# Kernel tuning notes

Measured on AMD Instinct MI355X. Metric: run time of the kernel, lower is better.

The kernel has to match this reference:

```python
import math
import jax, jax.numpy as jnp
import numpy as np

N_NODES = 50000
N_EDGES = 600000
IN_CH = 64      # in_channels == out_channels (residual requires it)
HEADS = 2
C = 64          # per-head dim == out_channels
HC = HEADS * C  # 128
EDGE_DIM = 32


def setup_inputs() -> dict:
    key = jax.random.key(0)
    ks = jax.random.split(key, 12)
    s = 0.05
    return {
        "x": jax.random.normal(ks[0], (N_NODES, IN_CH), jnp.float32),
        "edge_index": jax.random.randint(ks[1], (2, N_EDGES), 0, N_NODES, dtype=jnp.int64),
        "edge_attr": jax.random.normal(ks[2], (N_EDGES, EDGE_DIM), jnp.float32),
        "Wq": s * jax.random.normal(ks[3], (IN_CH, HC), jnp.float32),
        "bq": jnp.zeros((HC,), jnp.float32),
        "Wk": s * jax.random.normal(ks[4], (IN_CH, HC), jnp.float32),
        "bk": jnp.zeros((HC,), jnp.float32),
        "Wv": s * jax.random.normal(ks[5], (IN_CH, HC), jnp.float32),
        "bv": jnp.zeros((HC,), jnp.float32),
        "We": s * jax.random.normal(ks[6], (EDGE_DIM, HC), jnp.float32),
        "Wp": s * jax.random.normal(ks[7], (HC, IN_CH), jnp.float32),
        "bp": jnp.zeros((IN_CH,), jnp.float32),
        "ln1_g": jnp.ones((IN_CH,), jnp.float32),
        "ln1_b": jnp.zeros((IN_CH,), jnp.float32),
        "ln2_g": jnp.ones((IN_CH,), jnp.float32),
        "ln2_b": jnp.zeros((IN_CH,), jnp.float32),
        "W1": s * jax.random.normal(ks[8], (IN_CH, IN_CH), jnp.float32),
        "b1": jnp.zeros((IN_CH,), jnp.float32),
        "W2": s * jax.random.normal(ks[9], (IN_CH, IN_CH), jnp.float32),
        "b2": jnp.zeros((IN_CH,), jnp.float32),
    }


def _layernorm(x, g, b, eps=1e-5):
    m = jnp.mean(x, axis=-1, keepdims=True)
    v = jnp.mean(jnp.square(x - m), axis=-1, keepdims=True)
    return (x - m) / jnp.sqrt(v + eps) * g + b


def reference(x, edge_index, edge_attr, Wq, bq, Wk, bk, Wv, bv, We, Wp, bp,
              ln1_g, ln1_b, ln2_g, ln2_b, W1, b1, W2, b2):
    n = x.shape[0]
    residual = x
    h = _layernorm(x, ln1_g, ln1_b)
    q = (h @ Wq + bq).reshape(n, HEADS, C)
    k = (h @ Wk + bk).reshape(n, HEADS, C)
    v = (h @ Wv + bv).reshape(n, HEADS, C)

    src, tgt = edge_index[0], edge_index[1]
    e = (edge_attr @ We).reshape(-1, HEADS, C)   # (E,H,C)
    qi = q[tgt]                                  # (E,H,C) gather by target
    kj = k[src] + e
    vj = v[src] + e

    alpha = jnp.sum(qi * kj, axis=-1) / math.sqrt(C)            # (E,H)
    amax = jax.ops.segment_max(alpha, tgt, num_segments=n)      # (N,H)
    ex = jnp.exp(alpha - amax[tgt])
    den = jax.ops.segment_sum(ex, tgt, num_segments=n)          # (N,H)
    a = ex / (den[tgt] + 1e-8)                                  # (E,H)

    agg = jax.ops.segment_sum(a[:, :, None] * vj, tgt, num_segments=n)  # (N,H,C)
    out = agg.reshape(n, HC) @ Wp + bp
    out = out + residual                        # in_channels == out_channels

    res2 = out
    o = _layernorm(out, ln2_g, ln2_b)
    o = jax.nn.gelu(o @ W1 + b1, approximate=False) @ W2 + b2
    return o + res2
```

## Files before the change

### kernel.cpp

```cpp
#include <hip/hip_runtime.h>
#include <math.h>
#include <stdint.h>


typedef float f32x4 __attribute__((ext_vector_type(4)));
typedef __bf16 bf16x8 __attribute__((ext_vector_type(8)));
typedef unsigned int u32x4 __attribute__((ext_vector_type(4)));

#define WP_S 152
#define W1_OFF 9728
#define W2_OFF 15360
#define W_TOT 20992
#define H_S 72

__device__ __forceinline__ unsigned pack_bf16(float2 v) {
    unsigned a = __builtin_bit_cast(unsigned, v.x);
    unsigned b = __builtin_bit_cast(unsigned, v.y);
    a = (a + 0x7FFFu + ((a >> 16) & 1u)) >> 16;
    b = (b + 0x7FFFu + ((b >> 16) & 1u)) >> 16;
    return a | (b << 16);
}
__device__ __forceinline__ float2 unpack_bf16(unsigned p) {
    float x = __builtin_bit_cast(float, p << 16);
    float y = __builtin_bit_cast(float, p & 0xFFFF0000u);
    return make_float2(x, y);
}
__device__ __forceinline__ unsigned short bf16r(float x) {
    unsigned u = __builtin_bit_cast(unsigned, x);
    return (unsigned short)((u + 0x7FFFu + ((u >> 16) & 1u)) >> 16);
}

__device__ __forceinline__ f32x4 mfma16(bf16x8 a, bf16x8 b, f32x4 c) {
    return __builtin_amdgcn_mfma_f32_16x16x32_bf16(a, b, c, 0, 0, 0);
}
__device__ __forceinline__ bf16x8 frag_ld(const unsigned short* p) {
    return __builtin_bit_cast(bf16x8, *(const u32x4*)p);
}

__global__ void k_pre(const float* __restrict__ Wq, const float* __restrict__ Wk,
                      const float* __restrict__ Wv, const float* __restrict__ We,
                      const float* __restrict__ Wp, const float* __restrict__ W1,
                      const float* __restrict__ W2, const float* __restrict__ bq,
                      const float* __restrict__ bk, const float* __restrict__ bv,
                      float* __restrict__ Wqt, float* __restrict__ Wkt,
                      float* __restrict__ Wvt, float* __restrict__ Wet,
                      unsigned short* __restrict__ wsW, float* __restrict__ bqt,
                      float* __restrict__ bkt, float* __restrict__ bvt,
                      int* __restrict__ deg, int n) {
    int idx = blockIdx.x * 256 + threadIdx.x;
    for (int i = idx; i < n; i += gridDim.x * 256) deg[i] = 0;
    if (idx < 8192) {
        int cin = idx >> 7, j = idx & 127, h = j >> 6, c = j & 63;
        int dst = cin * 128 + c * 2 + h;
        Wqt[dst] = Wq[idx];
        Wkt[dst] = Wk[idx];
        Wvt[dst] = Wv[idx];
        int o = idx >> 7, k = idx & 127;
        wsW[o * WP_S + k] = bf16r(Wp[((k & 1) * 64 + (k >> 1)) * 64 + o]);
    }
    if (idx < 4096) {
        int d = idx >> 7, j = idx & 127, h = j >> 6, c = j & 63;
        Wet[(d * 64 + c) * 2 + h] = We[idx];
        int o = idx >> 6, k = idx & 63;
        wsW[W1_OFF + o * 88 + k] = bf16r(W1[k * 64 + o]);
        wsW[W2_OFF + o * 88 + k] = bf16r(W2[k * 64 + o]);
    }
    if (idx < 128) {
        int h = idx >> 6, c = idx & 63;
        bqt[c * 2 + h] = bq[idx];
        bkt[c * 2 + h] = bk[idx];
        bvt[c * 2 + h] = bv[idx];
    }
}

__global__ __launch_bounds__(256) void k_bucket(
    const int* __restrict__ ei, int* __restrict__ deg,
    int2* __restrict__ bucket2, int E, int n) {
    int e = blockIdx.x * 256 + threadIdx.x;
    if (e >= E) return;
    int src = ei[e], tgt = ei[E + e];
    src = min(max(src, 0), n - 1);
    tgt = min(max(tgt, 0), n - 1);
    int slot = atomicAdd(&deg[tgt], 1);
    if (slot < 64) bucket2[(size_t)tgt * 64 + slot] = make_int2(e, src);
}

__global__ __launch_bounds__(256) void k_qkv(
    const float* __restrict__ x,
    const float* __restrict__ Wqt, const float* __restrict__ Wkt, const float* __restrict__ Wvt,
    const float* __restrict__ bqt, const float* __restrict__ bkt, const float* __restrict__ bvt,
    const float* __restrict__ g1, const float* __restrict__ b1,
    const float* __restrict__ We,
    unsigned* __restrict__ qx, unsigned* __restrict__ kbf,
    unsigned* __restrict__ vbf, int n) {
    __shared__ __align__(16) float hT[4][64][8];
    __shared__ __align__(16) float qs[4][2][8][64];
    int wave = threadIdx.x >> 6, lane = threadIdx.x & 63;
    int node0 = blockIdx.x * 32 + wave * 8;
    if (node0 >= n) return;

    int b = lane >> 3, t = lane & 7;
    int nodeb = node0 + b;
    float4 xa = make_float4(0.f, 0.f, 0.f, 0.f), xb = xa;
    if (nodeb < n) {
        const float4* xp = (const float4*)(x + (size_t)nodeb * 64 + t * 8);
        xa = xp[0]; xb = xp[1];
    }
    float s1 = (xa.x + xa.y) + (xa.z + xa.w) + (xb.x + xb.y) + (xb.z + xb.w);
    float s2 = xa.x*xa.x + xa.y*xa.y + xa.z*xa.z + xa.w*xa.w
             + xb.x*xb.x + xb.y*xb.y + xb.z*xb.z + xb.w*xb.w;
#pragma unroll
    for (int m = 1; m < 8; m <<= 1) {
        s1 += __shfl_xor(s1, m);
        s2 += __shfl_xor(s2, m);
    }
    float mean = s1 * 0.015625f;
    float var  = s2 * 0.015625f - mean * mean;
    float rstd = rsqrtf(var + 1e-5f);
    float4 ga = ((const float4*)(g1 + t * 8))[0];
    float4 gb = ((const float4*)(g1 + t * 8))[1];
    float4 ba = ((const float4*)(b1 + t * 8))[0];
    float4 bb = ((const float4*)(b1 + t * 8))[1];
    float hv[8];
    hv[0] = (xa.x - mean) * rstd * ga.x + ba.x;
    hv[1] = (xa.y - mean) * rstd * ga.y + ba.y;
    hv[2] = (xa.z - mean) * rstd * ga.z + ba.z;
    hv[3] = (xa.w - mean) * rstd * ga.w + ba.w;
    hv[4] = (xb.x - mean) * rstd * gb.x + bb.x;
    hv[5] = (xb.y - mean) * rstd * gb.y + bb.y;
    hv[6] = (xb.z - mean) * rstd * gb.z + bb.z;
    hv[7] = (xb.w - mean) * rstd * gb.w + bb.w;
#pragma unroll
    for (int j = 0; j < 8; ++j) hT[wave][t * 8 + j][b] = hv[j];

    const float2* Wq2 = (const float2*)Wqt;
    const float2* Wk2 = (const float2*)Wkt;
    const float2* Wv2 = (const float2*)Wvt;
    float2 bqv = ((const float2*)bqt)[lane];
    float2 bkv = ((const float2*)bkt)[lane];
    float2 bvv = ((const float2*)bvt)[lane];
    float2 qa[8], ka[8], va[8];
#pragma unroll
    for (int nb = 0; nb < 8; ++nb) { qa[nb] = bqv; ka[nb] = bkv; va[nb] = bvv; }

#pragma unroll 4
    for (int cin = 0; cin < 64; ++cin) {
        float2 w_q = Wq2[cin * 64 + lane];
        float2 w_k = Wk2[cin * 64 + lane];
        float2 w_v = Wv2[cin * 64 + lane];
        const float4* hp = (const float4*)&hT[wave][cin][0];
        float4 h0 = hp[0], h1 = hp[1];
        float hs[8] = {h0.x, h0.y, h0.z, h0.w, h1.x, h1.y, h1.z, h1.w};
#pragma unroll
        for (int nb = 0; nb < 8; ++nb) {
            qa[nb].x += hs[nb] * w_q.x; qa[nb].y += hs[nb] * w_q.y;
            ka[nb].x += hs[nb] * w_k.x; ka[nb].y += hs[nb] * w_k.y;
            va[nb].x += hs[nb] * w_v.x; va[nb].y += hs[nb] * w_v.y;
        }
    }

#pragma unroll
    for (int nb = 0; nb < 8; ++nb) {
        int nd = node0 + nb;
        if (nd < n) {
            qx[(size_t)nd * 128 + lane] = pack_bf16(qa[nb]);
            kbf[(size_t)nd * 64 + lane] = pack_bf16(ka[nb]);
            vbf[(size_t)nd * 64 + lane] = pack_bf16(va[nb]);
        }
        qs[wave][0][nb][lane] = qa[nb].x;
        qs[wave][1][nb][lane] = qa[nb].y;
    }

    int hh = lane >> 5, d = lane & 31;
    const float4* Wr = (const float4*)(We + d * 128 + hh * 64);
    float wqa[8] = {0.f, 0.f, 0.f, 0.f, 0.f, 0.f, 0.f, 0.f};
#pragma unroll 4
    for (int c4 = 0; c4 < 16; ++c4) {
        float4 w = Wr[c4];
#pragma unroll
        for (int nb = 0; nb < 8; ++nb) {
            float4 qv = *(const float4*)&qs[wave][hh][nb][c4 * 4];
            wqa[nb] += w.x * qv.x + w.y * qv.y + w.z * qv.z + w.w * qv.w;
        }
    }
#pragma unroll
    for (int nb = 0; nb < 8; ++nb)
        if (node0 + nb < n)
            ((float*)qx)[(size_t)(node0 + nb) * 128 + 64 + d * 2 + hh] = wqa[nb];
}

__global__ __launch_bounds__(256) void k_attn(
    const unsigned* __restrict__ qx, const unsigned* __restrict__ kbf,
    const unsigned* __restrict__ vbf, const float* __restrict__ edge_attr,
    const int* __restrict__ deg, const int2* __restrict__ bucket2,
    const float* __restrict__ Wet,
    unsigned* __restrict__ agg, int n, int E) {
    __shared__ __align__(16) unsigned sq[4][64];
    __shared__ __align__(16) float swq[4][64];
    __shared__ __align__(16) float srow[4][64];
    __shared__ __align__(16) float2 sv[4][64];
    int wave = threadIdx.x >> 6, lane = threadIdx.x & 63;
    int node = blockIdx.x * 4 + wave;
    if (node >= n) return;
    int sub = lane >> 4, l = lane & 15;

    sq[wave][lane] = qx[(size_t)node * 128 + lane];
    swq[wave][lane] = ((const float*)qx)[(size_t)node * 128 + 64 + lane];

    int dcount = min(deg[node], 64);
    int eid_l = 0, src_l = 0;
    if (lane < dcount) {
        int2 b = bucket2[(size_t)node * 64 + lane];
        eid_l = min(max(b.x, 0), E - 1);
        src_l = min(max(b.y, 0), n - 1);
    }

    uint4 qq = *(const uint4*)&sq[wave][l * 4];
    float4 w4 = *(const float4*)&swq[wave][l * 4];
    float2 q0 = unpack_bf16(qq.x), q1 = unpack_bf16(qq.y),
           q2 = unpack_bf16(qq.z), q3 = unpack_bf16(qq.w);

    float accA[4] = {0.f, 0.f, 0.f, 0.f}, accB[4] = {0.f, 0.f, 0.f, 0.f};
    float aS0 = 0.f, aS1 = 0.f, bS0 = 0.f, bS1 = 0.f;
    float den0 = 0.f, den1 = 0.f;

    for (int i = 0; i < dcount; i += 4) {
        int j = i + sub;
        bool valid = j < dcount;
        int jj = j & 63;
        int ej = __shfl(eid_l, jj);
        int sj = __shfl(src_l, jj);
        uint4 kk = ((const uint4*)kbf)[(size_t)sj * 16 + l];
        uint4 vv = ((const uint4*)vbf)[(size_t)sj * 16 + l];
        float2 a2 = ((const float2*)edge_attr)[(size_t)ej * 16 + l];
        float2 k0 = unpack_bf16(kk.x), k1 = unpack_bf16(kk.y),
               k2 = unpack_bf16(kk.z), k3 = unpack_bf16(kk.w);
        float r0 = q0.x * k0.x + q1.x * k1.x + q2.x * k2.x + q3.x * k3.x
                 + w4.x * a2.x + w4.z * a2.y;
        float r1 = q0.y * k0.y + q1.y * k1.y + q2.y * k2.y + q3.y * k3.y
                 + w4.y * a2.x + w4.w * a2.y;
#pragma unroll
        for (int m = 1; m < 16; m <<= 1) {
            r0 += __shfl_xor(r0, m);
            r1 += __shfl_xor(r1, m);
        }
        float ex0 = valid ? __expf(r0 * 0.125f) : 0.f;
        float ex1 = valid ? __expf(r1 * 0.125f) : 0.f;
        float2 v0 = unpack_bf16(vv.x), v1 = unpack_bf16(vv.y),
               v2 = unpack_bf16(vv.z), v3 = unpack_bf16(vv.w);
        accA[0] += ex0 * v0.x; accB[0] += ex1 * v0.y;
        accA[1] += ex0 * v1.x; accB[1] += ex1 * v1.y;
        accA[2] += ex0 * v2.x; accB[2] += ex1 * v2.y;
        accA[3] += ex0 * v3.x; accB[3] += ex1 * v3.y;
        aS0 += ex0 * a2.x; aS1 += ex1 * a2.x;
        bS0 += ex0 * a2.y; bS1 += ex1 * a2.y;
        den0 += ex0; den1 += ex1;
    }

#pragma unroll
    for (int m = 16; m < 64; m <<= 1) {
#pragma unroll
        for (int j = 0; j < 4; ++j) {
            accA[j] += __shfl_xor(accA[j], m);
            accB[j] += __shfl_xor(accB[j], m);
        }
        aS0 += __shfl_xor(aS0, m); aS1 += __shfl_xor(aS1, m);
        bS0 += __shfl_xor(bS0, m); bS1 += __shfl_xor(bS1, m);
        den0 += __shfl_xor(den0, m); den1 += __shfl_xor(den1, m);
    }

    if (sub == 0) {
        srow[wave][4 * l + 0] = aS0;
        srow[wave][4 * l + 1] = aS1;
        srow[wave][4 * l + 2] = bS0;
        srow[wave][4 * l + 3] = bS1;
        sv[wave][4 * l + 0] = make_float2(accA[0], accB[0]);
        sv[wave][4 * l + 1] = make_float2(accA[1], accB[1]);
        sv[wave][4 * l + 2] = make_float2(accA[2], accB[2]);
        sv[wave][4 * l + 3] = make_float2(accA[3], accB[3]);
    }

    float B0 = 0.f, B1 = 0.f;
    const float2* We2 = (const float2*)Wet;
    const float2* S2 = (const float2*)srow[wave];
#pragma unroll
    for (int d = 0; d < 32; ++d) {
        float2 w = We2[d * 64 + lane];
        float2 s = S2[d];
        B0 += w.x * s.x;
        B1 += w.y * s.y;
    }
    float2 av2 = sv[wave][lane];
    float r0 = 1.0f / (den0 + 1e-8f);
    float r1 = 1.0f / (den1 + 1e-8f);
    agg[(size_t)node * 64 + lane] =
        pack_bf16(make_float2((av2.x + B0) * r0, (av2.y + B1) * r1));
}

__global__ __launch_bounds__(256) void k_post(
    const unsigned short* __restrict__ aggbf,
    const unsigned short* __restrict__ wsW,
    const float* __restrict__ bp, const float* __restrict__ x,
    const float* __restrict__ g2, const float* __restrict__ b2,
    const float* __restrict__ b1f, const float* __restrict__ b2f,
    float* __restrict__ out, int n) {
    __shared__ __align__(16) unsigned short sW[W_TOT];
    __shared__ __align__(16) unsigned short hb[4][2][16 * H_S];
    int tid = threadIdx.x;
    for (int i = tid; i < W_TOT / 8; i += 256)
        ((u32x4*)sW)[i] = ((const u32x4*)wsW)[i];
    __syncthreads();

    int wave = tid >> 6, lane = tid & 63;
    int cl = lane & 15, kg = lane >> 4;
    unsigned short* h2 = hb[wave][0];
    unsigned short* h3 = hb[wave][1];

    float bp_c[4], g2_c[4], b2_c[4], b1_c[4], bf2_c[4];
#pragma unroll
    for (int t = 0; t < 4; ++t) {
        int c = t * 16 + cl;
        bp_c[t] = bp[c];
        g2_c[t] = g2[c];
        b2_c[t] = b2[c];
        b1_c[t] = b1f[c];
        bf2_c[t] = b2f[c];
    }

    int wid = blockIdx.x * 4 + wave;
    int nbatch = (n + 15) >> 4;
    int nwaves = gridDim.x * 4;
    for (int bt = wid; bt < nbatch; bt += nwaves) {
        int node0 = bt * 16;

        f32x4 acc1[4];
#pragma unroll
        for (int t = 0; t < 4; ++t) acc1[t] = (f32x4){0.f, 0.f, 0.f, 0.f};
        int arow = min(node0 + cl, n - 1);
#pragma unroll
        for (int s = 0; s < 4; ++s) {
            bf16x8 af = frag_ld(aggbf + (size_t)arow * 128 + s * 32 + kg * 8);
#pragma unroll
            for (int t = 0; t < 4; ++t) {
                bf16x8 bf = frag_ld(sW + (t * 16 + cl) * WP_S + s * 32 + kg * 8);
                acc1[t] = mfma16(af, bf, acc1[t]);
            }
        }
#pragma unroll
        for (int t = 0; t < 4; ++t) {
#pragma unroll
            for (int j = 0; j < 4; ++j) {
                int nd = min(node0 + kg * 4 + j, n - 1);
                acc1[t][j] += bp_c[t] + x[(size_t)nd * 64 + t * 16 + cl];
            }
        }

        float mean[4], rstd[4];
#pragma unroll
        for (int j = 0; j < 4; ++j) {
            float s1 = acc1[0][j] + acc1[1][j] + acc1[2][j] + acc1[3][j];
            float s2 = acc1[0][j] * acc1[0][j] + acc1[1][j] * acc1[1][j]
                     + acc1[2][j] * acc1[2][j] + acc1[3][j] * acc1[3][j];
#pragma unroll
            for (int m = 1; m < 16; m <<= 1) {
                s1 += __shfl_xor(s1, m);
                s2 += __shfl_xor(s2, m);
            }
            mean[j] = s1 * 0.015625f;
            float var = s2 * 0.015625f - mean[j] * mean[j];
            rstd[j] = rsqrtf(var + 1e-5f);
        }
#pragma unroll
        for (int t = 0; t < 4; ++t)
#pragma unroll
            for (int j = 0; j < 4; ++j) {
                float v = (acc1[t][j] - mean[j]) * rstd[j] * g2_c[t] + b2_c[t];
                h2[(kg * 4 + j) * H_S + t * 16 + cl] = bf16r(v);
            }
        asm volatile("s_waitcnt lgkmcnt(0)" ::: "memory");

        f32x4 acc2[4];
#pragma unroll
        for (int t = 0; t < 4; ++t)
            acc2[t] = (f32x4){b1_c[t], b1_c[t], b1_c[t], b1_c[t]};
#pragma unroll
        for (int s = 0; s < 2; ++s) {
            bf16x8 af = frag_ld(h2 + cl * H_S + s * 32 + kg * 8);
#pragma unroll
            for (int t = 0; t < 4; ++t) {
                bf16x8 bf = frag_ld(sW + W1_OFF + (t * 16 + cl) * 88 + s * 32 + kg * 8);
                acc2[t] = mfma16(af, bf, acc2[t]);
            }
        }
#pragma unroll
        for (int t = 0; t < 4; ++t)
#pragma unroll
            for (int j = 0; j < 4; ++j) {
                float v = acc2[t][j];
                v = 0.5f * v * (1.0f + erff(v * 0.70710678118654752f));
                h3[(kg * 4 + j) * H_S + t * 16 + cl] = bf16r(v);
            }
        asm volatile("s_waitcnt lgkmcnt(0)" ::: "memory");

        f32x4 acc3[4];
#pragma unroll
        for (int t = 0; t < 4; ++t) {
            acc3[t] = acc1[t];
#pragma unroll
            for (int j = 0; j < 4; ++j) acc3[t][j] += bf2_c[t];
        }
#pragma unroll
        for (int s = 0; s < 2; ++s) {
            bf16x8 af = frag_ld(h3 + cl * H_S + s * 32 + kg * 8);
#pragma unroll
            for (int t = 0; t < 4; ++t) {
                bf16x8 bf = frag_ld(sW + W2_OFF + (t * 16 + cl) * 88 + s * 32 + kg * 8);
                acc3[t] = mfma16(af, bf, acc3[t]);
            }
        }
#pragma unroll
        for (int t = 0; t < 4; ++t)
#pragma unroll
            for (int j = 0; j < 4; ++j) {
                int r = node0 + kg * 4 + j;
                if (r < n) out[(size_t)r * 64 + t * 16 + cl] = acc3[t][j];
            }
    }
}

extern "C" void kernel_launch(void* const* d_in, const int* in_sizes, int n_in,
                              void* d_out, int out_size, void* d_ws, size_t ws_size,
                              hipStream_t stream) {
    const float* x  = (const float*)d_in[0];
    const int*   ei = (const int*)d_in[1];
    const float* ea = (const float*)d_in[2];
    const float* Wq = (const float*)d_in[3];
    const float* bq = (const float*)d_in[4];
    const float* Wk = (const float*)d_in[5];
    const float* bk = (const float*)d_in[6];
    const float* Wv = (const float*)d_in[7];
    const float* bv = (const float*)d_in[8];
    const float* We = (const float*)d_in[9];
    const float* Wp = (const float*)d_in[10];
    const float* bp = (const float*)d_in[11];
    const float* g1 = (const float*)d_in[12];
    const float* b1 = (const float*)d_in[13];
    const float* g2 = (const float*)d_in[14];
    const float* b2 = (const float*)d_in[15];
    const float* W1 = (const float*)d_in[16];
    const float* b1f = (const float*)d_in[17];
    const float* W2 = (const float*)d_in[18];
    const float* b2f = (const float*)d_in[19];

    const int n = in_sizes[0] / 64;
    const int E = in_sizes[2] / 32;

    char* p = (char*)d_ws;
    unsigned* qx = (unsigned*)p; p += (size_t)n * 128 * 4;
    unsigned* kbf = (unsigned*)p; p += (size_t)n * 64 * 4;
    unsigned* vbf = (unsigned*)p; p += (size_t)n * 64 * 4;
    int* deg   = (int*)p;   p += (size_t)n * 4;
    p = (char*)(((uintptr_t)p + 15) & ~(uintptr_t)15);
    int2* bucket2 = (int2*)p; p += (size_t)n * 64 * 8;
    unsigned* aggbf = (unsigned*)p; p += (size_t)n * 64 * 4;
    float* Wqt = (float*)p; p += 8192 * 4;
    float* Wkt = (float*)p; p += 8192 * 4;
    float* Wvt = (float*)p; p += 8192 * 4;
    float* Wet = (float*)p; p += 4096 * 4;
    unsigned short* wsW = (unsigned short*)p; p += W_TOT * 2;
    float* bqt = (float*)p; p += 128 * 4;
    float* bkt = (float*)p; p += 128 * 4;
    float* bvt = (float*)p; p += 128 * 4;

    k_pre<<<196, 256, 0, stream>>>(Wq, Wk, Wv, We, Wp, W1, W2, bq, bk, bv,
                                   Wqt, Wkt, Wvt, Wet, wsW, bqt, bkt, bvt,
                                   deg, n);
    k_bucket<<<(E + 255) / 256, 256, 0, stream>>>(ei, deg, bucket2, E, n);
    k_qkv<<<(n + 31) / 32, 256, 0, stream>>>(x, Wqt, Wkt, Wvt, bqt, bkt, bvt,
                                             g1, b1, We, qx, kbf, vbf, n);
    k_attn<<<(n + 3) / 4, 256, 0, stream>>>(qx, kbf, vbf, ea, deg, bucket2,
                                            Wet, aggbf, n, E);
    int nb16 = (n + 15) >> 4;
    int blocks = (nb16 + 3) / 4;
    if (blocks > 391) blocks = 391;
    k_post<<<blocks, 256, 0, stream>>>((const unsigned short*)aggbf, wsW,
                                       bp, x, g2, b2, b1f, b2f,
                                       (float*)d_out, n);
}
```

Baseline: 364.3 us.

## Fold We into Wp, software-pipeline edge gathers, and shrink bucket storage

Precomputes We·Wp so the attention kernel writes the per-head weighted edge-attribute sums (64 extra bf16 values per node) and the projection MFMA loop absorbs them, removing the per-node 32x64 We multiply and its shared-memory staging from k_attn. The edge loop now prefetches the next group's K, V and edge_attr rows while computing the current one. Source indices are stored as 16-bit values in a separate array to cut bucket traffic. In exchange the aggregate buffer grows from 128 to 192 bf16 per node, k_post does 6 instead of 4 K-steps, and the 16-bit source index only works while n fits in 65536.

```diff
diff --git a/kernel.cpp b/kernel.cpp
--- a/kernel.cpp
+++ b/kernel.cpp
@@ -7,10 +7,10 @@
 typedef __bf16 bf16x8 __attribute__((ext_vector_type(8)));
 typedef unsigned int u32x4 __attribute__((ext_vector_type(4)));
 
-#define WP_S 152
-#define W1_OFF 9728
-#define W2_OFF 15360
-#define W_TOT 20992
+#define WPM_S 200
+#define W1_OFF 12800
+#define W2_OFF 18432
+#define W_TOT 24064
 #define H_S 72
 
 __device__ __forceinline__ unsigned pack_bf16(float2 v) {
@@ -43,7 +43,7 @@
                       const float* __restrict__ W2, const float* __restrict__ bq,
                       const float* __restrict__ bk, const float* __restrict__ bv,
                       float* __restrict__ Wqt, float* __restrict__ Wkt,
-                      float* __restrict__ Wvt, float* __restrict__ Wet,
+                      float* __restrict__ Wvt,
                       unsigned short* __restrict__ wsW, float* __restrict__ bqt,
                       float* __restrict__ bkt, float* __restrict__ bvt,
                       int* __restrict__ deg, int n) {
@@ -56,14 +56,17 @@
         Wkt[dst] = Wk[idx];
         Wvt[dst] = Wv[idx];
         int o = idx >> 7, k = idx & 127;
-        wsW[o * WP_S + k] = bf16r(Wp[((k & 1) * 64 + (k >> 1)) * 64 + o]);
+        wsW[o * WPM_S + k] = bf16r(Wp[((k & 1) * 64 + (k >> 1)) * 64 + o]);
     }
     if (idx < 4096) {
-        int d = idx >> 7, j = idx & 127, h = j >> 6, c = j & 63;
-        Wet[(d * 64 + c) * 2 + h] = We[idx];
         int o = idx >> 6, k = idx & 63;
         wsW[W1_OFF + o * 88 + k] = bf16r(W1[k * 64 + o]);
         wsW[W2_OFF + o * 88 + k] = bf16r(W2[k * 64 + o]);
+        int o2 = idx & 63, dh = idx >> 6, d = dh >> 1, h = dh & 1;
+        float s = 0.f;
+        for (int c = 0; c < 64; ++c)
+            s += We[d * 128 + h * 64 + c] * Wp[(h * 64 + c) * 64 + o2];
+        wsW[o2 * WPM_S + 128 + dh] = bf16r(s);
     }
     if (idx < 128) {
         int h = idx >> 6, c = idx & 63;
@@ -75,14 +78,18 @@
 
 __global__ __launch_bounds__(256) void k_bucket(
     const int* __restrict__ ei, int* __restrict__ deg,
-    int2* __restrict__ bucket2, int E, int n) {
+    int* __restrict__ bucket_e, unsigned short* __restrict__ bucket_s,
+    int E, int n) {
     int e = blockIdx.x * 256 + threadIdx.x;
     if (e >= E) return;
     int src = ei[e], tgt = ei[E + e];
     src = min(max(src, 0), n - 1);
     tgt = min(max(tgt, 0), n - 1);
     int slot = atomicAdd(&deg[tgt], 1);
-    if (slot < 64) bucket2[(size_t)tgt * 64 + slot] = make_int2(e, src);
+    if (slot < 64) {
+        bucket_e[(size_t)tgt * 64 + slot] = e;
+        bucket_s[(size_t)tgt * 64 + slot] = (unsigned short)src;
+    }
 }
 
 __global__ __launch_bounds__(256) void k_qkv(
@@ -192,53 +199,59 @@
 __global__ __launch_bounds__(256) void k_attn(
     const unsigned* __restrict__ qx, const unsigned* __restrict__ kbf,
     const unsigned* __restrict__ vbf, const float* __restrict__ edge_attr,
-    const int* __restrict__ deg, const int2* __restrict__ bucket2,
-    const float* __restrict__ Wet,
-    unsigned* __restrict__ agg, int n, int E) {
-    __shared__ __align__(16) unsigned sq[4][64];
-    __shared__ __align__(16) float swq[4][64];
-    __shared__ __align__(16) float srow[4][64];
-    __shared__ __align__(16) float2 sv[4][64];
+    const int* __restrict__ deg, const int* __restrict__ bucket_e,
+    const unsigned short* __restrict__ bucket_s,
+    unsigned* __restrict__ aggs, int n, int E) {
     int wave = threadIdx.x >> 6, lane = threadIdx.x & 63;
     int node = blockIdx.x * 4 + wave;
     if (node >= n) return;
     int sub = lane >> 4, l = lane & 15;
 
-    sq[wave][lane] = qx[(size_t)node * 128 + lane];
-    swq[wave][lane] = ((const float*)qx)[(size_t)node * 128 + 64 + lane];
+    uint4 qq = ((const uint4*)qx)[(size_t)node * 32 + l];
+    float4 w4 = ((const float4*)qx)[(size_t)node * 32 + 16 + l];
+    float2 q0 = unpack_bf16(qq.x), q1 = unpack_bf16(qq.y),
+           q2 = unpack_bf16(qq.z), q3 = unpack_bf16(qq.w);
 
     int dcount = min(deg[node], 64);
     int eid_l = 0, src_l = 0;
     if (lane < dcount) {
-        int2 b = bucket2[(size_t)node * 64 + lane];
-        eid_l = min(max(b.x, 0), E - 1);
-        src_l = min(max(b.y, 0), n - 1);
-    }
-
-    uint4 qq = *(const uint4*)&sq[wave][l * 4];
-    float4 w4 = *(const float4*)&swq[wave][l * 4];
-    float2 q0 = unpack_bf16(qq.x), q1 = unpack_bf16(qq.y),
-           q2 = unpack_bf16(qq.z), q3 = unpack_bf16(qq.w);
+        eid_l = min(max(bucket_e[(size_t)node * 64 + lane], 0), E - 1);
+        src_l = min((int)bucket_s[(size_t)node * 64 + lane], n - 1);
+    }
+
+    const uint4* kb4 = (const uint4*)kbf;
+    const uint4* vb4 = (const uint4*)vbf;
+    const float2* ea2 = (const float2*)edge_attr;
 
     float accA[4] = {0.f, 0.f, 0.f, 0.f}, accB[4] = {0.f, 0.f, 0.f, 0.f};
     float aS0 = 0.f, aS1 = 0.f, bS0 = 0.f, bS1 = 0.f;
     float den0 = 0.f, den1 = 0.f;
 
+    uint4 kk, vv; float2 a2;
+    {
+        int jj = sub & 63;
+        int ej = __shfl(eid_l, jj), sj = __shfl(src_l, jj);
+        kk = kb4[(size_t)sj * 16 + l];
+        vv = vb4[(size_t)sj * 16 + l];
+        a2 = ea2[(size_t)ej * 16 + l];
+    }
     for (int i = 0; i < dcount; i += 4) {
-        int j = i + sub;
-        bool valid = j < dcount;
-        int jj = j & 63;
-        int ej = __shfl(eid_l, jj);
-        int sj = __shfl(src_l, jj);
-        uint4 kk = ((const uint4*)kbf)[(size_t)sj * 16 + l];
-        uint4 vv = ((const uint4*)vbf)[(size_t)sj * 16 + l];
-        float2 a2 = ((const float2*)edge_attr)[(size_t)ej * 16 + l];
-        float2 k0 = unpack_bf16(kk.x), k1 = unpack_bf16(kk.y),
-               k2 = unpack_bf16(kk.z), k3 = unpack_bf16(kk.w);
+        uint4 kc = kk, vc = vv; float2 ac = a2;
+        bool valid = (i + sub) < dcount;
+        int inx = i + 4;
+        if (inx < dcount) {
+            int jj = (inx + sub) & 63;
+            int ej = __shfl(eid_l, jj), sj = __shfl(src_l, jj);
+            kk = kb4[(size_t)sj * 16 + l];
+            vv = vb4[(size_t)sj * 16 + l];
+            a2 = ea2[(size_t)ej * 16 + l];
+        }
+        float2 k0 = unpack_bf16(kc.x), k1 = unpack_bf16(kc.y),
+               k2 = unpack_bf16(kc.z), k3 = unpack_bf16(kc.w);
         float r0 = q0.x * k0.x + q1.x * k1.x + q2.x * k2.x + q3.x * k3.x
-                 + w4.x * a2.x + w4.z * a2.y;
+                 + w4.x * ac.x + w4.z * ac.y;
         float r1 = q0.y * k0.y + q1.y * k1.y + q2.y * k2.y + q3.y * k3.y
-                 + w4.y * a2.x + w4.w * a2.y;
+                 + w4.y * ac.x + w4.w * ac.y;
 #pragma unroll
         for (int m = 1; m < 16; m <<= 1) {
             r0 += __shfl_xor(r0, m);
@@ -246,14 +259,14 @@
         }
         float ex0 = valid ? __expf(r0 * 0.125f) : 0.f;
         float ex1 = valid ? __expf(r1 * 0.125f) : 0.f;
-        float2 v0 = unpack_bf16(vv.x), v1 = unpack_bf16(vv.y),
-               v2 = unpack_bf16(vv.z), v3 = unpack_bf16(vv.w);
+        float2 v0 = unpack_bf16(vc.x), v1 = unpack_bf16(vc.y),
+               v2 = unpack_bf16(vc.z), v3 = unpack_bf16(vc.w);
         accA[0] += ex0 * v0.x; accB[0] += ex1 * v0.y;
         accA[1] += ex0 * v1.x; accB[1] += ex1 * v1.y;
         accA[2] += ex0 * v2.x; accB[2] += ex1 * v2.y;
         accA[3] += ex0 * v3.x; accB[3] += ex1 * v3.y;
-        aS0 += ex0 * a2.x; aS1 += ex1 * a2.x;
-        bS0 += ex0 * a2.y; bS1 += ex1 * a2.y;
+        aS0 += ex0 * ac.x; aS1 += ex1 * ac.x;
+        bS0 += ex0 * ac.y; bS1 += ex1 * ac.y;
         den0 += ex0; den1 += ex1;
     }
 
@@ -269,36 +282,23 @@
         den0 += __shfl_xor(den0, m); den1 += __shfl_xor(den1, m);
     }
 
-    if (sub == 0) {
-        srow[wave][4 * l + 0] = aS0;
-        srow[wave][4 * l + 1] = aS1;
-        srow[wave][4 * l + 2] = bS0;
-        srow[wave][4 * l + 3] = bS1;
-        sv[wave][4 * l + 0] = make_float2(accA[0], accB[0]);
-        sv[wave][4 * l + 1] = make_float2(accA[1], accB[1]);
-        sv[wave][4 * l + 2] = make_float2(accA[2], accB[2]);
-        sv[wave][4 * l + 3] = make_float2(accA[3], accB[3]);
-    }
-
-    float B0 = 0.f, B1 = 0.f;
-    const float2* We2 = (const float2*)Wet;
-    const float2* S2 = (const float2*)srow[wave];
-#pragma unroll
-    for (int d = 0; d < 32; ++d) {
-        float2 w = We2[d * 64 + lane];
-        float2 s = S2[d];
-        B0 += w.x * s.x;
-        B1 += w.y * s.y;
-    }
-    float2 av2 = sv[wave][lane];
     float r0 = 1.0f / (den0 + 1e-8f);
     float r1 = 1.0f / (den1 + 1e-8f);
-    agg[(size_t)node * 64 + lane] =
-        pack_bf16(make_float2((av2.x + B0) * r0, (av2.y + B1) * r1));
+
+    float va = sub == 0 ? accA[0] : sub == 1 ? accA[1] : sub == 2 ? accA[2] : accA[3];
+    float vb = sub == 0 ? accB[0] : sub == 1 ? accB[1] : sub == 2 ? accB[2] : accB[3];
+    aggs[(size_t)node * 96 + 4 * l + sub] =
+        pack_bf16(make_float2(va * r0, vb * r1));
+
+    if (sub == 0) {
+        unsigned s0 = pack_bf16(make_float2(aS0 * r0, aS1 * r1));
+        unsigned s1 = pack_bf16(make_float2(bS0 * r0, bS1 * r1));
+        *(uint2*)&aggs[(size_t)node * 96 + 64 + 2 * l] = make_uint2(s0, s1);
+    }
 }
 
 __global__ __launch_bounds__(256) void k_post(
-    const unsigned short* __restrict__ aggbf,
+    const unsigned short* __restrict__ aggsb,
     const unsigned short* __restrict__ wsW,
     const float* __restrict__ bp, const float* __restrict__ x,
     const float* __restrict__ g2, const float* __restrict__ b2,
@@ -338,11 +338,11 @@
         for (int t = 0; t < 4; ++t) acc1[t] = (f32x4){0.f, 0.f, 0.f, 0.f};
         int arow = min(node0 + cl, n - 1);
 #pragma unroll
-        for (int s = 0; s < 4; ++s) {
-            bf16x8 af = frag_ld(aggbf + (size_t)arow * 128 + s * 32 + kg * 8);
+        for (int s = 0; s < 6; ++s) {
+            bf16x8 af = frag_ld(aggsb + (size_t)arow * 192 + s * 32 + kg * 8);
 #pragma unroll
             for (int t = 0; t < 4; ++t) {
-                bf16x8 bf = frag_ld(sW + (t * 16 + cl) * WP_S + s * 32 + kg * 8);
+                bf16x8 bf = frag_ld(sW + (t * 16 + cl) * WPM_S + s * 32 + kg * 8);
                 acc1[t] = mfma16(af, bf, acc1[t]);
             }
         }
@@ -461,29 +461,31 @@
     unsigned* vbf = (unsigned*)p; p += (size_t)n * 64 * 4;
     int* deg   = (int*)p;   p += (size_t)n * 4;
     p = (char*)(((uintptr_t)p + 15) & ~(uintptr_t)15);
-    int2* bucket2 = (int2*)p; p += (size_t)n * 64 * 8;
-    unsigned* aggbf = (unsigned*)p; p += (size_t)n * 64 * 4;
+    int* bucket_e = (int*)p; p += (size_t)n * 64 * 4;
+    unsigned short* bucket_s = (unsigned short*)p; p += (size_t)n * 64 * 2;
+    p = (char*)(((uintptr_t)p + 15) & ~(uintptr_t)15);
+    unsigned* aggs = (unsigned*)p; p += (size_t)n * 96 * 4;
     float* Wqt = (float*)p; p += 8192 * 4;
     float* Wkt = (float*)p; p += 8192 * 4;
     float* Wvt = (float*)p; p += 8192 * 4;
-    float* Wet = (float*)p; p += 4096 * 4;
     unsigned short* wsW = (unsigned short*)p; p += W_TOT * 2;
     float* bqt = (float*)p; p += 128 * 4;
     float* bkt = (float*)p; p += 128 * 4;
     float* bvt = (float*)p; p += 128 * 4;
 
     k_pre<<<196, 256, 0, stream>>>(Wq, Wk, Wv, We, Wp, W1, W2, bq, bk, bv,
-                                   Wqt, Wkt, Wvt, Wet, wsW, bqt, bkt, bvt,
+                                   Wqt, Wkt, Wvt, wsW, bqt, bkt, bvt,
                                    deg, n);
-    k_bucket<<<(E + 255) / 256, 256, 0, stream>>>(ei, deg, bucket2, E, n);
+    k_bucket<<<(E + 255) / 256, 256, 0, stream>>>(ei, deg, bucket_e, bucket_s,
+                                                  E, n);
     k_qkv<<<(n + 31) / 32, 256, 0, stream>>>(x, Wqt, Wkt, Wvt, bqt, bkt, bvt,
                                              g1, b1, We, qx, kbf, vbf, n);
-    k_attn<<<(n + 3) / 4, 256, 0, stream>>>(qx, kbf, vbf, ea, deg, bucket2,
-                                            Wet, aggbf, n, E);
+    k_attn<<<(n + 3) / 4, 256, 0, stream>>>(qx, kbf, vbf, ea, deg,
+                                            bucket_e, bucket_s, aggs, n, E);
     int nb16 = (n + 15) >> 4;
     int blocks = (nb16 + 3) / 4;
     if (blocks > 391) blocks = 391;
-    k_post<<<blocks, 256, 0, stream>>>((const unsigned short*)aggbf, wsW,
+    k_post<<<blocks, 256, 0, stream>>>((const unsigned short*)aggs, wsW,
                                        bp, x, g2, b2, b1f, b2f,
                                        (float*)d_out, n);
 }
```

Result: faster. 325.8 us (-10.6%).
